# Kernel optimization log

Hardware: AMD Instinct MI355X
Metric: run time of the kernel (lower is better)

## Reference

```python
import jax, jax.numpy as jnp
import numpy as np

NIBBLES_PER_I32 = 8


def unpack_int4(q):
    """Unpack int32 [..., n] -> uint4 values in int32 [..., n*8], LSB-first."""
    shifts = (jnp.arange(NIBBLES_PER_I32, dtype=jnp.int32) * 4)
    nib = (q[..., None] >> shifts) & 0xF  # [..., n, 8]
    return nib.reshape(q.shape[:-1] + (q.shape[-1] * NIBBLES_PER_I32,))


def setup_inputs() -> dict:
    key = jax.random.key(0)
    k_x, k_w, k_z, k_s, k_b = jax.random.split(key, 5)
    B, S, IN, OUT, G = 2, 4096, 4096, 4096, 32
    x = jax.random.normal(k_x, (B, S, IN), dtype=jnp.float16)
    qweight = jax.random.randint(k_w, (OUT, IN // 8), 0, 2147483647, dtype=jnp.int32)
    qzeros = jax.random.randint(k_z, (G, OUT // 8), 0, 2147483647, dtype=jnp.int32)
    scales = (jax.random.uniform(k_s, (G, OUT), dtype=jnp.float32) * 0.01 + 0.001).astype(jnp.float16)
    bias = (jax.random.normal(k_b, (OUT,), dtype=jnp.float32) * 0.01).astype(jnp.float16)
    return {"x": x, "qweight": qweight, "qzeros": qzeros, "scales": scales, "bias": bias}


def reference(x, qweight, qzeros, scales, bias):
    # GPTQ W4A16: dequantize int4 weight with per-group scales/zero-points, then GEMM + bias.
    x = x.astype(jnp.float16)
    wq = unpack_int4(qweight)            # [out, in] int4 values
    zq = unpack_int4(qzeros)             # [groups, out]
    out_f, in_f = wq.shape
    G = scales.shape[0]
    gsize = in_f // G
    wq_g = wq.reshape(out_f, G, gsize)                       # [out, G, gsize]
    zero = zq.T.astype(jnp.float16)[:, :, None]              # [out, G, 1]
    scale = scales.T.astype(jnp.float16)[:, :, None]         # [out, G, 1]
    w = ((wq_g.astype(jnp.float16) - zero) * scale).reshape(out_f, in_f)  # [out, in] fp16
    y = jnp.einsum("bsi,oi->bso", x, w)                     # [B, S, out]
    return y + bias
```

## Files before the change

kernel.cpp:

```cpp
#include <hip/hip_runtime.h>
#include <cstdint>

typedef unsigned short u16;
typedef unsigned int   u32;
typedef unsigned long long u64;

typedef _Float16 f16x2 __attribute__((ext_vector_type(2)));
typedef _Float16 f16x8 __attribute__((ext_vector_type(8)));
typedef float    f32x4 __attribute__((ext_vector_type(4)));

__device__ __forceinline__ u32 cvt_pk(float a, float b) {
    return __builtin_bit_cast(u32, __builtin_amdgcn_cvt_pkrtz(a, b));
}

__device__ __forceinline__ f16x8 unpack_dq(u32 q, f16x2 cz, f16x2 cs) {
    const u32 b0 = (q & 0x000F000Fu) | 0x64006400u;
    const u32 b1 = ((q >> 4) & 0x000F000Fu) | 0x64006400u;
    const u32 b2 = ((q >> 8) & 0x000F000Fu) | 0x64006400u;
    const u32 b3 = ((q >> 12) & 0x000F000Fu) | 0x64006400u;
    const f16x2 w0 = (__builtin_bit_cast(f16x2, b0) - cz) * cs;
    const f16x2 w1 = (__builtin_bit_cast(f16x2, b1) - cz) * cs;
    const f16x2 w2 = (__builtin_bit_cast(f16x2, b2) - cz) * cs;
    const f16x2 w3 = (__builtin_bit_cast(f16x2, b3) - cz) * cs;
    uint4 w;
    w.x = __builtin_bit_cast(u32, w0);
    w.y = __builtin_bit_cast(u32, w1);
    w.z = __builtin_bit_cast(u32, w2);
    w.w = __builtin_bit_cast(u32, w3);
    return __builtin_bit_cast(f16x8, w);
}

__device__ __forceinline__ void load_lds16(const void* g, void* l) {
    __builtin_amdgcn_global_load_lds(
        (const __attribute__((address_space(1))) void*)g,
        (__attribute__((address_space(3))) void*)l,
        16, 0, 0);
}

__global__ __launch_bounds__(256) void gptq_prepass(
    const float* __restrict__ X, u16* __restrict__ Xh)
{
    const u32 tile = blockIdx.x;
    const u32 mt = tile >> 6, t = tile & 63;
    const float* bsrc = X + ((u64)mt << 19) + t * 64;
    u16* bdst = Xh + ((u64)tile << 13);
#pragma unroll
    for (int pass = 0; pass < 4; ++pass) {
        const u32 idx = pass * 256 + threadIdx.x;
        const u32 r = idx >> 3, sg = idx & 7, g = sg ^ (r & 7);
        const float* s = bsrc + ((u64)r << 12) + g * 8;
        const float4 f0 = *(const float4*)s;
        const float4 f1 = *(const float4*)(s + 4);
        uint4 w;
        w.x = cvt_pk(f0.x, f1.x);
        w.y = cvt_pk(f0.y, f1.y);
        w.z = cvt_pk(f0.z, f1.z);
        w.w = cvt_pk(f0.w, f1.w);
        *(uint4*)(bdst + idx * 8) = w;
    }
}

__global__ __launch_bounds__(256) void gptq_transpose(
    const int* __restrict__ QW, int* __restrict__ QWt)
{
    __shared__ int tile[64][65];
    const u32 bkq = blockIdx.x;
    const u32 bn  = blockIdx.y;
    const u32 t = threadIdx.x;
    const u32 r = t >> 4, c4 = (t & 15) * 4;
#pragma unroll
    for (int p = 0; p < 4; ++p) {
        const u32 row = p * 16 + r;
        const int4 v = *(const int4*)(QW + (u64)(bn * 64 + row) * 512
                                         + bkq * 64 + c4);
        tile[row][c4 + 0] = v.x; tile[row][c4 + 1] = v.y;
        tile[row][c4 + 2] = v.z; tile[row][c4 + 3] = v.w;
    }
    __syncthreads();
#pragma unroll
    for (int p = 0; p < 4; ++p) {
        const u32 kql = p * 16 + r;
        int4 v;
        v.x = tile[c4 + 0][kql]; v.y = tile[c4 + 1][kql];
        v.z = tile[c4 + 2][kql]; v.w = tile[c4 + 3][kql];
        *(int4*)(QWt + (u64)(bkq * 64 + kql) * 4096 + bn * 64 + c4) = v;
    }
}

__global__ __launch_bounds__(256, 2) void gptq_gemm_dma(
    const u16* __restrict__ Xh,
    const int* __restrict__ QWt,
    const int* __restrict__ QZ,
    const float* __restrict__ SC,
    const float* __restrict__ BIAS,
    float* __restrict__ Y)
{
    constexpr int N = 4096, NT = 64;

    __shared__ __align__(16) u16 Alds[2][128 * 64];

    const int tid  = threadIdx.x;
    const int lane = tid & 63;
    const int wid  = tid >> 6;

    const int mt = blockIdx.x;
    const int m0 = mt * 128;
    const int n0 = blockIdx.y * 256;

    f32x4 acc[8][4];
#pragma unroll
    for (int i = 0; i < 8; i++)
#pragma unroll
        for (int j = 0; j < 4; j++)
            acc[i][j] = (f32x4){0.f, 0.f, 0.f, 0.f};

    const int fr   = lane & 15;
    const int quad = lane >> 4;
    const int fr7  = fr & 7;

    const char* xsrc = (const char*)Xh + (((u64)mt * NT) << 14)
                     + wid * 4096 + lane * 16;

    const int nbase = n0 + wid * 64 + fr;
    const char* QWtB = (const char*)QWt;
    const u64 qtbase = (u64)((u32)(quad * 4096 + nbase) * 4u);

    int   bq[2][8];
    float sf_st[4];
    int   zw_st[4];
    f16x2 cs[4], cz[4];
    const int zsh = fr7 * 4;

    auto STAGE = [&](int buf, int t) {
        const char* s = xsrc + ((u64)t << 14);
        char* d = (char*)&Alds[buf][0] + wid * 4096;
#pragma unroll
        for (int i = 0; i < 4; i++)
            load_lds16(s + i * 1024, d + i * 1024);
    };

    auto FETCH_B = [&](int t, int nb) {
        const char* p = QWtB + ((u64)t << 17) + qtbase;
#pragma unroll
        for (int ni = 0; ni < 4; ni++) {
            bq[nb][ni * 2 + 0] = *(const int*)(p + ni * 64);
            bq[nb][ni * 2 + 1] = *(const int*)(p + 65536 + ni * 64);
        }
    };

    auto FETCH_SZ = [&](int g) {
#pragma unroll
        for (int ni = 0; ni < 4; ni++) {
            sf_st[ni] = SC[g * N + nbase + ni * 16];
            zw_st[ni] = QZ[g * (N / 8) + ((nbase + ni * 16) >> 3)];
        }
    };

    auto CONV_SZ = [&]() {
#pragma unroll
        for (int ni = 0; ni < 4; ni++) {
            const int z = (zw_st[ni] >> zsh) & 0xF;
            const _Float16 hs = (_Float16)sf_st[ni];
            const _Float16 hz = (_Float16)(float)(1024 + z);
            cs[ni] = (f16x2){hs, hs};
            cz[ni] = (f16x2){hz, hz};
        }
    };

    auto COMPUTE = [&](int buf, int nb) {
#pragma unroll
        for (int ks = 0; ks < 2; ks++) {
            f16x8 bfr[4];
#pragma unroll
            for (int ni = 0; ni < 4; ni++)
                bfr[ni] = unpack_dq((u32)bq[nb][ni * 2 + ks], cz[ni], cs[ni]);
            const int gsw = ((ks * 4 + quad) ^ fr7) * 8;
            __builtin_amdgcn_s_setprio(1);
#pragma unroll
            for (int mi = 0; mi < 8; mi++) {
                const f16x8 af =
                    *(const f16x8*)(&Alds[buf][(mi * 16 + fr) * 64 + gsw]);
#pragma unroll
                for (int ni = 0; ni < 4; ni++)
                    acc[mi][ni] = __builtin_amdgcn_mfma_f32_16x16x32_f16(
                        af, bfr[ni], acc[mi][ni], 0, 0, 0);
            }
            __builtin_amdgcn_s_setprio(0);
        }
    };

    FETCH_B(0, 0);
    FETCH_SZ(0);
    STAGE(0, 0);
    STAGE(1, 1);
    CONV_SZ();
    asm volatile("s_waitcnt vmcnt(4)\n\ts_barrier" ::: "memory");

    for (int t = 0; t <= 60; t += 2) {
        FETCH_B(t + 1, 1);
        FETCH_SZ((t >> 1) + 1);
        COMPUTE(0, 0);
        asm volatile("s_barrier" ::: "memory");
        STAGE(0, t + 2);
        asm volatile("s_waitcnt vmcnt(20)\n\ts_barrier" ::: "memory");

        FETCH_B(t + 2, 0);
        COMPUTE(1, 1);
        CONV_SZ();
        asm volatile("s_barrier" ::: "memory");
        STAGE(1, t + 3);
        asm volatile("s_waitcnt vmcnt(12)\n\ts_barrier" ::: "memory");
    }

    FETCH_B(63, 1);
    COMPUTE(0, 0);
    asm volatile("s_waitcnt vmcnt(8)\n\ts_barrier" ::: "memory");
    COMPUTE(1, 1);

    const int cn  = lane & 15;
    const int q4r = quad * 4;
#pragma unroll
    for (int ni = 0; ni < 4; ni++) {
        const int col = n0 + wid * 64 + ni * 16 + cn;
        const float bz = BIAS[col];
#pragma unroll
        for (int mi = 0; mi < 8; mi++) {
            const int rbase = m0 + mi * 16 + q4r;
#pragma unroll
            for (int r = 0; r < 4; r++) {
                Y[(u64)(rbase + r) * N + col] = acc[mi][ni][r] + bz;
            }
        }
    }
}

__global__ __launch_bounds__(256, 2) void gptq_gemm_fb(
    const float* __restrict__ X, const int* __restrict__ QW,
    const int* __restrict__ QZ, const float* __restrict__ SC,
    const float* __restrict__ BIAS, float* __restrict__ Y)
{
    constexpr int N = 4096, K = 4096, KB = 512, NT = 64;
    __shared__ __align__(16) u16 Alds[2][128 * 64];
    __shared__ __align__(16) u16 Blds[2][128 * 64];

    const int tid = threadIdx.x, lane = tid & 63, wid = tid >> 6;
    const int m0 = blockIdx.x * 128, n0 = blockIdx.y * 128;

    f32x4 acc[4][4];
#pragma unroll
    for (int i = 0; i < 4; i++)
#pragma unroll
        for (int j = 0; j < 4; j++) acc[i][j] = (f32x4){0.f, 0.f, 0.f, 0.f};

    const int wm = (wid >> 1) * 64, wn = (wid & 1) * 64;
    const int lrowA = tid >> 3;
    const float* gA = X + (u64)(m0 + lrowA) * K + (tid & 7) * 8;
    const int sA = ((tid & 7) ^ (lrowA & 7)) * 8;
    const int nl = tid >> 1, kq0 = (tid & 1) * 4;
    const int nglob = n0 + nl;
    const int* qrow = QW + (u64)nglob * KB;
    const int nl7 = nl & 7, zsh = (nglob & 7) * 4;
    const float* scp = SC + nglob;
    const int* qzp = QZ + (nglob >> 3);
    const int fr = lane & 15, quad = lane >> 4, fr7 = fr & 7;

    float4 af32[8];
    int4 q4;
    float sf;
    int zw;

    auto FETCH = [&](int t) {
        const int kt = t * 64;
#pragma unroll
        for (int i = 0; i < 4; i++) {
            const float* pa = gA + (u64)i * 32 * K + kt;
            af32[2 * i] = *(const float4*)pa;
            af32[2 * i + 1] = *(const float4*)(pa + 4);
        }
        q4 = *(const int4*)(qrow + (kt >> 3) + kq0);
        const int g = t >> 1;
        sf = scp[g * N];
        zw = qzp[g * (N / 8)];
    };
    auto STORE = [&](int buf) {
#pragma unroll
        for (int i = 0; i < 4; i++) {
            const float4 f0 = af32[2 * i], f1 = af32[2 * i + 1];
            uint4 w;
            w.x = cvt_pk(f0.x, f1.x); w.y = cvt_pk(f0.y, f1.y);
            w.z = cvt_pk(f0.z, f1.z); w.w = cvt_pk(f0.w, f1.w);
            *(uint4*)(&Alds[buf][(i * 32 + lrowA) * 64 + sA]) = w;
        }
        const int z = (zw >> zsh) & 0xF;
        const _Float16 hs = (_Float16)sf;
        const _Float16 hz = (_Float16)(float)(1024 + z);
        const f16x2 cs2 = {hs, hs}, cz2 = {hz, hz};
        const int qv[4] = {q4.x, q4.y, q4.z, q4.w};
#pragma unroll
        for (int c = 0; c < 4; c++) {
            const f16x8 wv = unpack_dq((u32)qv[c], cz2, cs2);
            const int gran = ((kq0 + c) ^ nl7) * 8;
            *(f16x8*)(&Blds[buf][nl * 64 + gran]) = wv;
        }
    };
    auto COMPUTE = [&](int buf) {
#pragma unroll
        for (int ks = 0; ks < 2; ks++) {
            const int gsw = ((ks * 4 + quad) ^ fr7) * 8;
            f16x8 af[4], bfr[4];
#pragma unroll
            for (int i = 0; i < 4; i++)
                af[i] = *(const f16x8*)(&Alds[buf][(wm + i * 16 + fr) * 64 + gsw]);
#pragma unroll
            for (int i = 0; i < 4; i++)
                bfr[i] = *(const f16x8*)(&Blds[buf][(wn + i * 16 + fr) * 64 + gsw]);
#pragma unroll
            for (int mi = 0; mi < 4; mi++)
#pragma unroll
                for (int ni = 0; ni < 4; ni++)
                    acc[mi][ni] = __builtin_amdgcn_mfma_f32_16x16x32_f16(
                        af[mi], bfr[ni], acc[mi][ni], 0, 0, 0);
        }
    };

    FETCH(0); STORE(0); __syncthreads();
#pragma unroll 2
    for (int t = 0; t < NT; ++t) {
        const int cur = t & 1;
        if (t + 1 < NT) FETCH(t + 1);
        COMPUTE(cur);
        if (t + 1 < NT) STORE(cur ^ 1);
        __syncthreads();
    }
    const int cn = lane & 15, q4r = quad * 4;
#pragma unroll
    for (int ni = 0; ni < 4; ni++) {
        const int col = n0 + wn + ni * 16 + cn;
        const float bz = BIAS[col];
#pragma unroll
        for (int mi = 0; mi < 4; mi++) {
            const int rbase = m0 + wm + mi * 16 + q4r;
#pragma unroll
            for (int r = 0; r < 4; r++)
                Y[(u64)(rbase + r) * N + col] = acc[mi][ni][r] + bz;
        }
    }
}

extern "C" void kernel_launch(void* const* d_in, const int* in_sizes, int n_in,
                              void* d_out, int out_size, void* d_ws, size_t ws_size,
                              hipStream_t stream) {
    const float* X    = (const float*)d_in[0];
    const int*   QW   = (const int*)d_in[1];
    const int*   QZ   = (const int*)d_in[2];
    const float* SC   = (const float*)d_in[3];
    const float* BIAS = (const float*)d_in[4];
    float* Y = (float*)d_out;

    const size_t needXh = (size_t)8192 * 4096 * sizeof(u16);
    const size_t needAll = needXh + (size_t)512 * 4096 * 4;
    if (ws_size >= needAll) {
        u16* Xh  = (u16*)d_ws;
        int* QWt = (int*)((char*)d_ws + needXh);
        gptq_prepass<<<4096, 256, 0, stream>>>(X, Xh);
        gptq_transpose<<<dim3(8, 64), 256, 0, stream>>>(QW, QWt);
        dim3 grid(64, 16, 1);
        gptq_gemm_dma<<<grid, 256, 0, stream>>>(Xh, QWt, QZ, SC, BIAS, Y);
    } else {
        dim3 grid(64, 32, 1);
        gptq_gemm_fb<<<grid, 256, 0, stream>>>(X, QW, QZ, SC, BIAS, Y);
    }
}
```

Measured before the change: 480.3 us.

## Dequantize weights to fp16 in a prepass and feed a plain fp16 GEMM

Adds a prepass kernel that transposes the int4 weights, dequantizes them with the per-group scale and zero-point, and writes fp16 B fragments into a workspace laid out in MFMA register order. A new GEMM kernel then loads these fp16 fragments directly and drops all in-loop unpacking and scale/zero fetches. This takes the dequant ALU work off the MFMA critical path. In exchange, B memory traffic grows fourfold (a 32 MB fp16 matrix is reread by every M tile instead of 8 MB int4), the dequant pass writes that matrix once, and the path needs a larger workspace.

```diff
diff --git a/kernel.cpp b/kernel.cpp
--- a/kernel.cpp
+++ b/kernel.cpp
@@ -60,8 +60,9 @@
     }
 }
 
-__global__ __launch_bounds__(256) void gptq_transpose(
-    const int* __restrict__ QW, int* __restrict__ QWt)
+__global__ __launch_bounds__(256) void gptq_dequantB(
+    const int* __restrict__ QW, const int* __restrict__ QZ,
+    const float* __restrict__ SC, u16* __restrict__ Bt)
 {
     __shared__ int tile[64][65];
     const u32 bkq = blockIdx.x;
@@ -77,6 +78,159 @@
         tile[row][c4 + 2] = v.z; tile[row][c4 + 3] = v.w;
     }
     __syncthreads();
+    char* BtB = (char*)Bt;
+#pragma unroll
+    for (int p = 0; p < 4; ++p) {
+        const u32 kql = p * 16 + r;
+        const u32 chunk = bkq * 64 + kql;
+        const u32 g = chunk >> 4;
+        const u32 quad = chunk & 3;
+        const u64 base = ((u64)((chunk >> 2) * 256)) * 1024 + quad * 256;
+#pragma unroll
+        for (int e = 0; e < 4; ++e) {
+            const u32 n = bn * 64 + c4 + e;
+            const u32 q = (u32)tile[c4 + e][kql];
+            const float s = SC[g * 4096 + n];
+            const int zw = QZ[g * 512 + (n >> 3)];
+            const int z = (zw >> ((n & 7) * 4)) & 0xF;
+            const _Float16 hs = (_Float16)s;
+            const _Float16 hz = (_Float16)(float)(1024 + z);
+            const f16x8 v = unpack_dq(q, (f16x2){hz, hz}, (f16x2){hs, hs});
+            *(f16x8*)(BtB + base + (u64)(n >> 4) * 1024 + (n & 15) * 16) = v;
+        }
+    }
+}
+
+__global__ __launch_bounds__(256, 2) void gptq_gemm_dq(
+    const u16* __restrict__ Xh,
+    const u16* __restrict__ Bt,
+    const float* __restrict__ BIAS,
+    float* __restrict__ Y)
+{
+    constexpr int N = 4096, NT = 64;
+
+    __shared__ __align__(16) u16 Alds[2][128 * 64];
+
+    const int tid  = threadIdx.x;
+    const int lane = tid & 63;
+    const int wid  = tid >> 6;
+
+    const int mt = blockIdx.x;
+    const int m0 = mt * 128;
+    const int n0 = blockIdx.y * 256;
+
+    f32x4 acc[8][4];
+#pragma unroll
+    for (int i = 0; i < 8; i++)
+#pragma unroll
+        for (int j = 0; j < 4; j++)
+            acc[i][j] = (f32x4){0.f, 0.f, 0.f, 0.f};
+
+    const int fr   = lane & 15;
+    const int quad = lane >> 4;
+    const int fr7  = fr & 7;
+
+    const char* xsrc = (const char*)Xh + (((u64)mt * NT) << 14)
+                     + wid * 4096 + lane * 16;
+
+    const int nb16 = (n0 >> 4) + wid * 4;
+    const char* btb = (const char*)Bt + (u64)nb16 * 1024 + lane * 16;
+
+    f16x8 bq[2][2][4];
+
+    auto STAGE = [&](int buf, int t) {
+        const char* s = xsrc + ((u64)t << 14);
+        char* d = (char*)&Alds[buf][0] + wid * 4096;
+#pragma unroll
+        for (int i = 0; i < 4; i++)
+            load_lds16(s + i * 1024, d + i * 1024);
+    };
+
+    auto FETCH_B = [&](int t, int nb) {
+#pragma unroll
+        for (int ks = 0; ks < 2; ks++) {
+            const char* p = btb + ((u64)(t * 2 + ks) << 18);
+#pragma unroll
+            for (int ni = 0; ni < 4; ni++)
+                bq[nb][ks][ni] = *(const f16x8*)(p + ni * 1024);
+        }
+    };
+
+    auto COMPUTE = [&](int buf, int nb) {
+#pragma unroll
+        for (int ks = 0; ks < 2; ks++) {
+            const int gsw = ((ks * 4 + quad) ^ fr7) * 8;
+            __builtin_amdgcn_s_setprio(1);
+#pragma unroll
+            for (int mi = 0; mi < 8; mi++) {
+                const f16x8 af =
+                    *(const f16x8*)(&Alds[buf][(mi * 16 + fr) * 64 + gsw]);
+#pragma unroll
+                for (int ni = 0; ni < 4; ni++)
+                    acc[mi][ni] = __builtin_amdgcn_mfma_f32_16x16x32_f16(
+                        af, bq[nb][ks][ni], acc[mi][ni], 0, 0, 0);
+            }
+            __builtin_amdgcn_s_setprio(0);
+        }
+    };
+
+    FETCH_B(0, 0);
+    STAGE(0, 0);
+    STAGE(1, 1);
+    asm volatile("s_waitcnt vmcnt(4)\n\ts_barrier" ::: "memory");
+
+    for (int t = 0; t <= 60; t += 2) {
+        FETCH_B(t + 1, 1);
+        COMPUTE(0, 0);
+        asm volatile("s_barrier" ::: "memory");
+        STAGE(0, t + 2);
+        asm volatile("s_waitcnt vmcnt(12)\n\ts_barrier" ::: "memory");
+
+        FETCH_B(t + 2, 0);
+        COMPUTE(1, 1);
+        asm volatile("s_barrier" ::: "memory");
+        STAGE(1, t + 3);
+        asm volatile("s_waitcnt vmcnt(12)\n\ts_barrier" ::: "memory");
+    }
+
+    FETCH_B(63, 1);
+    COMPUTE(0, 0);
+    asm volatile("s_waitcnt vmcnt(8)\n\ts_barrier" ::: "memory");
+    COMPUTE(1, 1);
+
+    const int cn  = lane & 15;
+    const int q4r = quad * 4;
+#pragma unroll
+    for (int ni = 0; ni < 4; ni++) {
+        const int col = n0 + wid * 64 + ni * 16 + cn;
+        const float bz = BIAS[col];
+#pragma unroll
+        for (int mi = 0; mi < 8; mi++) {
+            const int rbase = m0 + mi * 16 + q4r;
+#pragma unroll
+            for (int r = 0; r < 4; r++) {
+                Y[(u64)(rbase + r) * N + col] = acc[mi][ni][r] + bz;
+            }
+        }
+    }
+}
+
+__global__ __launch_bounds__(256) void gptq_transpose(
+    const int* __restrict__ QW, int* __restrict__ QWt)
+{
+    __shared__ int tile[64][65];
+    const u32 bkq = blockIdx.x, bn = blockIdx.y;
+    const u32 t = threadIdx.x;
+    const u32 r = t >> 4, c4 = (t & 15) * 4;
+#pragma unroll
+    for (int p = 0; p < 4; ++p) {
+        const u32 row = p * 16 + r;
+        const int4 v = *(const int4*)(QW + (u64)(bn * 64 + row) * 512
+                                         + bkq * 64 + c4);
+        tile[row][c4 + 0] = v.x; tile[row][c4 + 1] = v.y;
+        tile[row][c4 + 2] = v.z; tile[row][c4 + 3] = v.w;
+    }
+    __syncthreads();
 #pragma unroll
     for (int p = 0; p < 4; ++p) {
         const u32 kql = p * 16 + r;
@@ -88,57 +242,36 @@
 }
 
 __global__ __launch_bounds__(256, 2) void gptq_gemm_dma(
-    const u16* __restrict__ Xh,
-    const int* __restrict__ QWt,
-    const int* __restrict__ QZ,
-    const float* __restrict__ SC,
-    const float* __restrict__ BIAS,
-    float* __restrict__ Y)
+    const u16* __restrict__ Xh, const int* __restrict__ QWt,
+    const int* __restrict__ QZ, const float* __restrict__ SC,
+    const float* __restrict__ BIAS, float* __restrict__ Y)
 {
     constexpr int N = 4096, NT = 64;
-
     __shared__ __align__(16) u16 Alds[2][128 * 64];
-
-    const int tid  = threadIdx.x;
-    const int lane = tid & 63;
-    const int wid  = tid >> 6;
-
-    const int mt = blockIdx.x;
-    const int m0 = mt * 128;
-    const int n0 = blockIdx.y * 256;
-
+    const int tid = threadIdx.x, lane = tid & 63, wid = tid >> 6;
+    const int mt = blockIdx.x, m0 = mt * 128, n0 = blockIdx.y * 256;
     f32x4 acc[8][4];
 #pragma unroll
     for (int i = 0; i < 8; i++)
 #pragma unroll
-        for (int j = 0; j < 4; j++)
-            acc[i][j] = (f32x4){0.f, 0.f, 0.f, 0.f};
-
-    const int fr   = lane & 15;
-    const int quad = lane >> 4;
-    const int fr7  = fr & 7;
-
+        for (int j = 0; j < 4; j++) acc[i][j] = (f32x4){0.f, 0.f, 0.f, 0.f};
+    const int fr = lane & 15, quad = lane >> 4, fr7 = fr & 7;
     const char* xsrc = (const char*)Xh + (((u64)mt * NT) << 14)
                      + wid * 4096 + lane * 16;
-
     const int nbase = n0 + wid * 64 + fr;
     const char* QWtB = (const char*)QWt;
     const u64 qtbase = (u64)((u32)(quad * 4096 + nbase) * 4u);
-
-    int   bq[2][8];
+    int bq[2][8];
     float sf_st[4];
-    int   zw_st[4];
+    int zw_st[4];
     f16x2 cs[4], cz[4];
     const int zsh = fr7 * 4;
-
     auto STAGE = [&](int buf, int t) {
         const char* s = xsrc + ((u64)t << 14);
         char* d = (char*)&Alds[buf][0] + wid * 4096;
 #pragma unroll
-        for (int i = 0; i < 4; i++)
-            load_lds16(s + i * 1024, d + i * 1024);
-    };
-
+        for (int i = 0; i < 4; i++) load_lds16(s + i * 1024, d + i * 1024);
+    };
     auto FETCH_B = [&](int t, int nb) {
         const char* p = QWtB + ((u64)t << 17) + qtbase;
 #pragma unroll
@@ -147,7 +280,6 @@
             bq[nb][ni * 2 + 1] = *(const int*)(p + 65536 + ni * 64);
         }
     };
-
     auto FETCH_SZ = [&](int g) {
 #pragma unroll
         for (int ni = 0; ni < 4; ni++) {
@@ -155,7 +287,6 @@
             zw_st[ni] = QZ[g * (N / 8) + ((nbase + ni * 16) >> 3)];
         }
     };
-
     auto CONV_SZ = [&]() {
 #pragma unroll
         for (int ni = 0; ni < 4; ni++) {
@@ -166,7 +297,6 @@
             cz[ni] = (f16x2){hz, hz};
         }
     };
-
     auto COMPUTE = [&](int buf, int nb) {
 #pragma unroll
         for (int ks = 0; ks < 2; ks++) {
@@ -188,14 +318,12 @@
             __builtin_amdgcn_s_setprio(0);
         }
     };
-
     FETCH_B(0, 0);
     FETCH_SZ(0);
     STAGE(0, 0);
     STAGE(1, 1);
     CONV_SZ();
     asm volatile("s_waitcnt vmcnt(4)\n\ts_barrier" ::: "memory");
-
     for (int t = 0; t <= 60; t += 2) {
         FETCH_B(t + 1, 1);
         FETCH_SZ((t >> 1) + 1);
@@ -203,7 +331,6 @@
         asm volatile("s_barrier" ::: "memory");
         STAGE(0, t + 2);
         asm volatile("s_waitcnt vmcnt(20)\n\ts_barrier" ::: "memory");
-
         FETCH_B(t + 2, 0);
         COMPUTE(1, 1);
         CONV_SZ();
@@ -211,14 +338,11 @@
         STAGE(1, t + 3);
         asm volatile("s_waitcnt vmcnt(12)\n\ts_barrier" ::: "memory");
     }
-
     FETCH_B(63, 1);
     COMPUTE(0, 0);
     asm volatile("s_waitcnt vmcnt(8)\n\ts_barrier" ::: "memory");
     COMPUTE(1, 1);
-
-    const int cn  = lane & 15;
-    const int q4r = quad * 4;
+    const int cn = lane & 15, q4r = quad * 4;
 #pragma unroll
     for (int ni = 0; ni < 4; ni++) {
         const int col = n0 + wid * 64 + ni * 16 + cn;
@@ -227,9 +351,8 @@
         for (int mi = 0; mi < 8; mi++) {
             const int rbase = m0 + mi * 16 + q4r;
 #pragma unroll
-            for (int r = 0; r < 4; r++) {
+            for (int r = 0; r < 4; r++)
                 Y[(u64)(rbase + r) * N + col] = acc[mi][ni][r] + bz;
-            }
         }
     }
 }
@@ -242,16 +365,13 @@
     constexpr int N = 4096, K = 4096, KB = 512, NT = 64;
     __shared__ __align__(16) u16 Alds[2][128 * 64];
     __shared__ __align__(16) u16 Blds[2][128 * 64];
-
     const int tid = threadIdx.x, lane = tid & 63, wid = tid >> 6;
     const int m0 = blockIdx.x * 128, n0 = blockIdx.y * 128;
-
     f32x4 acc[4][4];
 #pragma unroll
     for (int i = 0; i < 4; i++)
 #pragma unroll
         for (int j = 0; j < 4; j++) acc[i][j] = (f32x4){0.f, 0.f, 0.f, 0.f};
-
     const int wm = (wid >> 1) * 64, wn = (wid & 1) * 64;
     const int lrowA = tid >> 3;
     const float* gA = X + (u64)(m0 + lrowA) * K + (tid & 7) * 8;
@@ -263,12 +383,10 @@
     const float* scp = SC + nglob;
     const int* qzp = QZ + (nglob >> 3);
     const int fr = lane & 15, quad = lane >> 4, fr7 = fr & 7;
-
     float4 af32[8];
     int4 q4;
     float sf;
     int zw;
-
     auto FETCH = [&](int t) {
         const int kt = t * 64;
 #pragma unroll
@@ -322,7 +440,6 @@
                         af[mi], bfr[ni], acc[mi][ni], 0, 0, 0);
         }
     };
-
     FETCH(0); STORE(0); __syncthreads();
 #pragma unroll 2
     for (int t = 0; t < NT; ++t) {
@@ -358,8 +475,16 @@
     float* Y = (float*)d_out;
 
     const size_t needXh = (size_t)8192 * 4096 * sizeof(u16);
-    const size_t needAll = needXh + (size_t)512 * 4096 * 4;
-    if (ws_size >= needAll) {
+    const size_t needNew = needXh + (size_t)4096 * 4096 * 2;
+    const size_t needMid = needXh + (size_t)512 * 4096 * 4;
+    if (ws_size >= needNew) {
+        u16* Xh = (u16*)d_ws;
+        u16* Bt = (u16*)((char*)d_ws + needXh);
+        gptq_prepass<<<4096, 256, 0, stream>>>(X, Xh);
+        gptq_dequantB<<<dim3(8, 64), 256, 0, stream>>>(QW, QZ, SC, Bt);
+        dim3 grid(64, 16, 1);
+        gptq_gemm_dq<<<grid, 256, 0, stream>>>(Xh, Bt, BIAS, Y);
+    } else if (ws_size >= needMid) {
         u16* Xh  = (u16*)d_ws;
         int* QWt = (int*)((char*)d_ws + needXh);
         gptq_prepass<<<4096, 256, 0, stream>>>(X, Xh);
```

Result: no change. 480.8 us (+0.1%).
